# Kernel tuning notes

Hardware: AMD Instinct MI355X
Metric: run time of the kernel (lower is better)

Reference implementation:

```python
import jax, jax.numpy as jnp
import numpy as np
from jax import lax

KERNEL = 3
SAMPLING_RATE = 100.0
N_GRID = 201  # np.linspace(-1, 1, 201) sub-sample grid


def setup_inputs() -> dict:
    key = jax.random.key(0)
    nb, nc, nx, nt = 32, 3, 64, 4096
    xcorr = jax.random.normal(key, (nb, nc, nx, nt), dtype=jnp.float32)
    return {"xcorr": xcorr, "nlag": nt // 2}


def reference(xcorr, nlag):
    nt = xcorr.shape[-1]
    x = jnp.abs(xcorr)  # vabs=True

    # max_pool2d with (1, kernel=3), stride 1, padding (0, 1) -> SAME max over lag axis
    smax = lax.reduce_window(
        x, -jnp.inf, lax.max,
        window_dimensions=(1, 1, 1, KERNEL),
        window_strides=(1, 1, 1, 1),
        padding=[(0, 0), (0, 0), (0, 0), (KERNEL // 2, KERNEL // 2)],
    )
    keep = (smax == x).astype(x.dtype)

    # top-2 local maxima along lag axis (sorted descending, like torch.topk)
    topk_score, topk_idx = lax.top_k(x * keep, 2)
    s0 = topk_score[..., 0]
    s1 = topk_score[..., 1]
    weight = (0.1 + 3.0 * (s0 - s1)) * s0 ** 2
    i0 = topk_idx[..., 0]  # [nb, nc, nx]

    # --- sub-sample interpolation: 3-point spline == parabola through neighbors ---
    offsets = jnp.array([-1, 0, 1], dtype=i0.dtype)
    nbr_idx = jnp.clip(i0[..., None] + offsets, 0, nt - 1)      # [nb,nc,nx,3]
    y = jnp.take_along_axis(x, nbr_idx, axis=-1)                 # [nb,nc,nx,3]
    ym1, y0, yp1 = y[..., 0], y[..., 1], y[..., 2]
    a = 0.5 * (ym1 + yp1) - y0   # quadratic coeff
    b = 0.5 * (yp1 - ym1)        # linear coeff
    c = y0                       # constant

    xg = jnp.linspace(-1.0, 1.0, N_GRID, dtype=x.dtype)          # [201]
    yg = (a[..., None] * xg + b[..., None]) * xg + c[..., None]  # [nb,nc,nx,201]
    ii = jnp.argmax(yg, axis=-1)                                  # [nb,nc,nx]
    sub_shift = xg[ii]
    topk_idx_f = i0.astype(x.dtype) + sub_shift
    topk_score0 = jnp.take_along_axis(yg, ii[..., None], axis=-1)[..., 0]

    # pick the channel with the largest weight
    idx = jnp.argmax(weight, axis=1, keepdims=True)               # [nb,1,nx]
    max_cc = jnp.take_along_axis(topk_score0, idx, axis=1)
    w = jnp.take_along_axis(weight, idx, axis=1)
    shift_idx = jnp.take_along_axis(topk_idx_f, idx, axis=1) - jnp.asarray(nlag, x.dtype)
    shift_t = shift_idx / SAMPLING_RATE

    # stacked: [cc_max, cc_weight, cc_dt, cc_shift], each [nb,1,nx]
    return jnp.stack([max_cc, w, shift_t, shift_idx], axis=0)
```

## Files before the change

### kernel.cpp

```cpp
#include <hip/hip_runtime.h>
#include <math.h>

#define NB 32
#define NC 3
#define NX 64
#define NT 4096
#define NROWS (NB * NC * NX)

struct Quad { float4 a, b, c, d; };

__device__ __forceinline__ Quad load_chunk(const float* __restrict__ xr,
                                           int coff, int lane) {
    const float* base = xr + (size_t)coff + (size_t)(lane << 2);
    Quad q;
    q.a = *reinterpret_cast<const float4*>(base);
    q.b = *reinterpret_cast<const float4*>(base + 256);
    q.c = *reinterpret_cast<const float4*>(base + 512);
    q.d = *reinterpret_cast<const float4*>(base + 768);
    return q;
}

__device__ __forceinline__ void proc4(float a0, float a1, float a2, float a3,
                                      float cl, float cr, int t4,
                                      float& v0, int& i0, float& v1)
{
    const float c0 = (a0 >= cl && a0 >= a1) ? a0 : 0.0f;
    const float c1 = (a1 >= a0 && a1 >= a2) ? a1 : 0.0f;
    const float c2 = (a2 >= a1 && a2 >= a3) ? a2 : 0.0f;
    const float c3 = (a3 >= a2 && a3 >= cr) ? a3 : 0.0f;
    bool g;
    g = c0 > v0; v1 = g ? v0 : fmaxf(v1, c0); v0 = fmaxf(v0, c0); i0 = g ? t4     : i0;
    g = c1 > v0; v1 = g ? v0 : fmaxf(v1, c1); v0 = fmaxf(v0, c1); i0 = g ? t4 + 1 : i0;
    g = c2 > v0; v1 = g ? v0 : fmaxf(v1, c2); v0 = fmaxf(v0, c2); i0 = g ? t4 + 2 : i0;
    g = c3 > v0; v1 = g ? v0 : fmaxf(v1, c3); v0 = fmaxf(v0, c3); i0 = g ? t4 + 3 : i0;
}

__device__ __forceinline__ void scan_chunk(Quad q, float lmf, float rmf,
                                           int coff, int lane,
                                           float& v0, int& i0, float& v1)
{
    const int base = coff + (lane << 2);

    const float a00 = fabsf(q.a.x), a01 = fabsf(q.a.y), a02 = fabsf(q.a.z), a03 = fabsf(q.a.w);
    const float a10 = fabsf(q.b.x), a11 = fabsf(q.b.y), a12 = fabsf(q.b.z), a13 = fabsf(q.b.w);
    const float a20 = fabsf(q.c.x), a21 = fabsf(q.c.y), a22 = fabsf(q.c.z), a23 = fabsf(q.c.w);
    const float a30 = fabsf(q.d.x), a31 = fabsf(q.d.y), a32 = fabsf(q.d.z), a33 = fabsf(q.d.w);

    float lm, rm, t;

    lm = __shfl_up(a03, 1);
    lm = (lane == 0) ? lmf : lm;
    rm = __shfl_down(a00, 1);
    t  = __shfl(a10, 0);
    rm = (lane == 63) ? t : rm;
    proc4(a00, a01, a02, a03, lm, rm, base, v0, i0, v1);

    lm = __shfl_up(a13, 1);
    t  = __shfl(a03, 63);
    lm = (lane == 0) ? t : lm;
    rm = __shfl_down(a10, 1);
    t  = __shfl(a20, 0);
    rm = (lane == 63) ? t : rm;
    proc4(a10, a11, a12, a13, lm, rm, base + 256, v0, i0, v1);

    lm = __shfl_up(a23, 1);
    t  = __shfl(a13, 63);
    lm = (lane == 0) ? t : lm;
    rm = __shfl_down(a20, 1);
    t  = __shfl(a30, 0);
    rm = (lane == 63) ? t : rm;
    proc4(a20, a21, a22, a23, lm, rm, base + 512, v0, i0, v1);

    lm = __shfl_up(a33, 1);
    t  = __shfl(a23, 63);
    lm = (lane == 0) ? t : lm;
    rm = __shfl_down(a30, 1);
    rm = (lane == 63) ? rmf : rm;
    proc4(a30, a31, a32, a33, lm, rm, base + 768, v0, i0, v1);
}

__global__ __launch_bounds__(256) void scan_rows_kernel(
    const float* __restrict__ xcorr,
    float* __restrict__ wsv0, int* __restrict__ wsi0, float* __restrict__ wsv1)
{
    const int tid  = threadIdx.x;
    const int lane = tid & 63;
    const int wid  = tid >> 6;
    const int row  = blockIdx.x * 4 + wid;

    const float* __restrict__ xr = xcorr + (size_t)row * NT;

    float v0 = -1.0f, v1 = -1.0f; int i0 = 0;
    float pl, nf;

    Quad qA = load_chunk(xr, 0, lane);
    Quad qB = load_chunk(xr, 1024, lane);

    nf = __shfl(fabsf(qB.a.x), 0);
    scan_chunk(qA, -INFINITY, nf, 0, lane, v0, i0, v1);
    pl = __shfl(fabsf(qA.d.w), 63);

    qA = load_chunk(xr, 2048, lane);
    nf = __shfl(fabsf(qA.a.x), 0);
    scan_chunk(qB, pl, nf, 1024, lane, v0, i0, v1);
    pl = __shfl(fabsf(qB.d.w), 63);

    qB = load_chunk(xr, 3072, lane);
    nf = __shfl(fabsf(qB.a.x), 0);
    scan_chunk(qA, pl, nf, 2048, lane, v0, i0, v1);
    pl = __shfl(fabsf(qA.d.w), 63);

    scan_chunk(qB, pl, -INFINITY, 3072, lane, v0, i0, v1);

    #pragma unroll
    for (int off = 1; off < 64; off <<= 1) {
        const float ov0 = __shfl_xor(v0, off);
        const int   oi0 = __shfl_xor(i0, off);
        const float ov1 = __shfl_xor(v1, off);
        const bool big = (ov0 > v0) || (ov0 == v0 && oi0 < i0);
        const float loser = big ? v0 : ov0;
        v1 = fmaxf(fmaxf(v1, ov1), loser);
        v0 = big ? ov0 : v0;
        i0 = big ? oi0 : i0;
    }

    if (lane == 0) {
        wsv0[row] = v0;
        wsi0[row] = i0;
        wsv1[row] = v1;
    }
}

__global__ __launch_bounds__(256) void epilogue_kernel(
    const float* __restrict__ xcorr,
    const float* __restrict__ wsv0, const int* __restrict__ wsi0,
    const float* __restrict__ wsv1,
    const int*   __restrict__ nlag_p,
    float* __restrict__ out)
{
    const int g = blockIdx.x * 256 + threadIdx.x;
    if (g >= NB * NX) return;
    const int b = g >> 6;
    const int x = g & 63;

    const int r0 = (b * NC + 0) * NX + x;
    const int r1 = (b * NC + 1) * NX + x;
    const int r2 = (b * NC + 2) * NX + x;

    const float m00 = wsv0[r0], m10 = wsv1[r0]; const int p0 = wsi0[r0];
    const float m01 = wsv0[r1], m11 = wsv1[r1]; const int p1 = wsi0[r1];
    const float m02 = wsv0[r2], m12 = wsv1[r2]; const int p2 = wsi0[r2];

    const float w0 = (0.1f + 3.0f * (m00 - m10)) * (m00 * m00);
    const float w1 = (0.1f + 3.0f * (m01 - m11)) * (m01 * m01);
    const float w2 = (0.1f + 3.0f * (m02 - m12)) * (m02 * m02);

    const bool t1 = w1 > w0;
    float bw = t1 ? w1 : w0;
    float bs = t1 ? m01 : m00;
    int   bp = t1 ? p1 : p0;
    int   rs = t1 ? r1 : r0;
    const bool t2 = w2 > bw;
    bw = t2 ? w2 : bw;
    bs = t2 ? m02 : bs;
    bp = t2 ? p2 : bp;
    rs = t2 ? r2 : rs;

    const float* __restrict__ xrs = xcorr + (size_t)rs * NT;

    const float ym1 = fabsf(xrs[bp > 0 ? bp - 1 : 0]);
    const float yp1 = fabsf(xrs[bp < NT - 1 ? bp + 1 : NT - 1]);
    const float A = 0.5f * (ym1 + yp1) - bs;
    const float B = 0.5f * (yp1 - ym1);
    const float C = bs;

    int gi; float bv;
    if (A == 0.0f) {
        gi = (B > 0.0f) ? 200 : 0;
        const float xg = 0.01f * (float)(gi - 100);
        bv = (A * xg + B) * xg + C;
    } else {
        float gv = (1.0f - 0.5f * B / A) * 100.0f;
        gv = fminf(fmaxf(gv, 0.0f), 200.0f);
        const int glo = (int)gv;
        bv = -INFINITY; gi = 0;
        #pragma unroll
        for (int d = -1; d <= 2; ++d) {
            int gg = glo + d;
            gg = gg < 0 ? 0 : (gg > 200 ? 200 : gg);
            const float xg = 0.01f * (float)(gg - 100);
            const float yg = (A * xg + B) * xg + C;
            if (yg > bv) { bv = yg; gi = gg; }
        }
    }

    const float fidx = (float)bp + 0.01f * (float)(gi - 100);
    const float nlagf = (float)(*nlag_p);
    const float shift_idx = fidx - nlagf;
    const int n = NB * NX;
    out[0 * n + g] = bv;
    out[1 * n + g] = bw;
    out[2 * n + g] = shift_idx / 100.0f;
    out[3 * n + g] = shift_idx;
}

extern "C" void kernel_launch(void* const* d_in, const int* in_sizes, int n_in,
                              void* d_out, int out_size, void* d_ws, size_t ws_size,
                              hipStream_t stream) {
    const float* xcorr  = (const float*)d_in[0];
    const int*   nlag_p = (const int*)d_in[1];
    float* out = (float*)d_out;

    float* ws   = (float*)d_ws;
    float* wsv0 = ws;
    int*   wsi0 = (int*)(ws + NROWS);
    float* wsv1 = ws + 2 * NROWS;

    scan_rows_kernel<<<NROWS / 4, 256, 0, stream>>>(xcorr, wsv0, wsi0, wsv1);

    epilogue_kernel<<<(NB * NX + 255) / 256, 256, 0, stream>>>(
        xcorr, wsv0, wsi0, wsv1, nlag_p, out);
}
```

Measured before the change: 25.01 us.

## Give each lane 16 contiguous samples and split top-2 accumulators into four chains

Each lane now loads 16 contiguous floats per 1024-sample chunk instead of four strided float4s. This drops most cross-lane shuffles for neighbor values to one shuffle up and one down per chunk. All four chunks are loaded up front, and each chunk keeps its own top-2 accumulator so the dependency chains are independent; the accumulators are merged at the end. Lanes now read 64-byte contiguous segments rather than fully coalesced 16-byte strided ones, and holding all four chunks in flight raises register pressure.

```diff
diff --git a/kernel.cpp b/kernel.cpp
--- a/kernel.cpp
+++ b/kernel.cpp
@@ -9,74 +9,71 @@
 
 struct Quad { float4 a, b, c, d; };
 
-__device__ __forceinline__ Quad load_chunk(const float* __restrict__ xr,
-                                           int coff, int lane) {
-    const float* base = xr + (size_t)coff + (size_t)(lane << 2);
+__device__ __forceinline__ Quad load_chunk16(const float* __restrict__ xr,
+                                             int coff, int lane) {
+    const float* base = xr + (size_t)coff + (size_t)(lane << 4);
     Quad q;
     q.a = *reinterpret_cast<const float4*>(base);
-    q.b = *reinterpret_cast<const float4*>(base + 256);
-    q.c = *reinterpret_cast<const float4*>(base + 512);
-    q.d = *reinterpret_cast<const float4*>(base + 768);
+    q.b = *reinterpret_cast<const float4*>(base + 4);
+    q.c = *reinterpret_cast<const float4*>(base + 8);
+    q.d = *reinterpret_cast<const float4*>(base + 12);
     return q;
 }
 
-__device__ __forceinline__ void proc4(float a0, float a1, float a2, float a3,
-                                      float cl, float cr, int t4,
-                                      float& v0, int& i0, float& v1)
-{
-    const float c0 = (a0 >= cl && a0 >= a1) ? a0 : 0.0f;
-    const float c1 = (a1 >= a0 && a1 >= a2) ? a1 : 0.0f;
-    const float c2 = (a2 >= a1 && a2 >= a3) ? a2 : 0.0f;
-    const float c3 = (a3 >= a2 && a3 >= cr) ? a3 : 0.0f;
-    bool g;
-    g = c0 > v0; v1 = g ? v0 : fmaxf(v1, c0); v0 = fmaxf(v0, c0); i0 = g ? t4     : i0;
-    g = c1 > v0; v1 = g ? v0 : fmaxf(v1, c1); v0 = fmaxf(v0, c1); i0 = g ? t4 + 1 : i0;
-    g = c2 > v0; v1 = g ? v0 : fmaxf(v1, c2); v0 = fmaxf(v0, c2); i0 = g ? t4 + 2 : i0;
-    g = c3 > v0; v1 = g ? v0 : fmaxf(v1, c3); v0 = fmaxf(v0, c3); i0 = g ? t4 + 3 : i0;
-}
-
-__device__ __forceinline__ void scan_chunk(Quad q, float lmf, float rmf,
-                                           int coff, int lane,
-                                           float& v0, int& i0, float& v1)
-{
-    const int base = coff + (lane << 2);
-
-    const float a00 = fabsf(q.a.x), a01 = fabsf(q.a.y), a02 = fabsf(q.a.z), a03 = fabsf(q.a.w);
-    const float a10 = fabsf(q.b.x), a11 = fabsf(q.b.y), a12 = fabsf(q.b.z), a13 = fabsf(q.b.w);
-    const float a20 = fabsf(q.c.x), a21 = fabsf(q.c.y), a22 = fabsf(q.c.z), a23 = fabsf(q.c.w);
-    const float a30 = fabsf(q.d.x), a31 = fabsf(q.d.y), a32 = fabsf(q.d.z), a33 = fabsf(q.d.w);
-
-    float lm, rm, t;
-
-    lm = __shfl_up(a03, 1);
-    lm = (lane == 0) ? lmf : lm;
-    rm = __shfl_down(a00, 1);
-    t  = __shfl(a10, 0);
-    rm = (lane == 63) ? t : rm;
-    proc4(a00, a01, a02, a03, lm, rm, base, v0, i0, v1);
-
-    lm = __shfl_up(a13, 1);
-    t  = __shfl(a03, 63);
-    lm = (lane == 0) ? t : lm;
-    rm = __shfl_down(a10, 1);
-    t  = __shfl(a20, 0);
-    rm = (lane == 63) ? t : rm;
-    proc4(a10, a11, a12, a13, lm, rm, base + 256, v0, i0, v1);
-
-    lm = __shfl_up(a23, 1);
-    t  = __shfl(a13, 63);
-    lm = (lane == 0) ? t : lm;
-    rm = __shfl_down(a20, 1);
-    t  = __shfl(a30, 0);
-    rm = (lane == 63) ? t : rm;
-    proc4(a20, a21, a22, a23, lm, rm, base + 512, v0, i0, v1);
-
-    lm = __shfl_up(a33, 1);
-    t  = __shfl(a23, 63);
-    lm = (lane == 0) ? t : lm;
-    rm = __shfl_down(a30, 1);
-    rm = (lane == 63) ? rmf : rm;
-    proc4(a30, a31, a32, a33, lm, rm, base + 768, v0, i0, v1);
+__device__ __forceinline__ float keep3(float l, float x, float r) {
+    const float m = fmaxf(fmaxf(l, x), r);
+    return (x == m) ? x : 0.0f;
+}
+
+__device__ __forceinline__ void ins(float c, int t, float& m0, int& i0, float& m1) {
+    const bool g = c > m0;
+    m1 = g ? m0 : fmaxf(m1, c);
+    m0 = fmaxf(m0, c);
+    i0 = g ? t : i0;
+}
+
+__device__ __forceinline__ void scan_chunk16(Quad q, float lmE, float rmE,
+                                             int coff, int lane,
+                                             float& m0, int& i0, float& m1)
+{
+    const int tb = coff + (lane << 4);
+
+    const float e0  = fabsf(q.a.x), e1  = fabsf(q.a.y), e2  = fabsf(q.a.z), e3  = fabsf(q.a.w);
+    const float e4  = fabsf(q.b.x), e5  = fabsf(q.b.y), e6  = fabsf(q.b.z), e7  = fabsf(q.b.w);
+    const float e8  = fabsf(q.c.x), e9  = fabsf(q.c.y), e10 = fabsf(q.c.z), e11 = fabsf(q.c.w);
+    const float e12 = fabsf(q.d.x), e13 = fabsf(q.d.y), e14 = fabsf(q.d.z), e15 = fabsf(q.d.w);
+
+    float lm = __shfl_up(e15, 1);
+    lm = (lane == 0) ? lmE : lm;
+    float rm = __shfl_down(e0, 1);
+    rm = (lane == 63) ? rmE : rm;
+
+    ins(keep3(lm,  e0,  e1 ), tb + 0,  m0, i0, m1);
+    ins(keep3(e0,  e1,  e2 ), tb + 1,  m0, i0, m1);
+    ins(keep3(e1,  e2,  e3 ), tb + 2,  m0, i0, m1);
+    ins(keep3(e2,  e3,  e4 ), tb + 3,  m0, i0, m1);
+    ins(keep3(e3,  e4,  e5 ), tb + 4,  m0, i0, m1);
+    ins(keep3(e4,  e5,  e6 ), tb + 5,  m0, i0, m1);
+    ins(keep3(e5,  e6,  e7 ), tb + 6,  m0, i0, m1);
+    ins(keep3(e6,  e7,  e8 ), tb + 7,  m0, i0, m1);
+    ins(keep3(e7,  e8,  e9 ), tb + 8,  m0, i0, m1);
+    ins(keep3(e8,  e9,  e10), tb + 9,  m0, i0, m1);
+    ins(keep3(e9,  e10, e11), tb + 10, m0, i0, m1);
+    ins(keep3(e10, e11, e12), tb + 11, m0, i0, m1);
+    ins(keep3(e11, e12, e13), tb + 12, m0, i0, m1);
+    ins(keep3(e12, e13, e14), tb + 13, m0, i0, m1);
+    ins(keep3(e13, e14, e15), tb + 14, m0, i0, m1);
+    ins(keep3(e14, e15, rm ), tb + 15, m0, i0, m1);
+}
+
+__device__ __forceinline__ void merge_acc(float& m0, int& i0, float& m1,
+                                          float bm0, int bi0, float bm1)
+{
+    const bool big = bm0 > m0;
+    const float loser = big ? m0 : bm0;
+    m1 = fmaxf(fmaxf(m1, bm1), loser);
+    m0 = big ? bm0 : m0;
+    i0 = big ? bi0 : i0;
 }
 
 __global__ __launch_bounds__(256) void scan_rows_kernel(
@@ -90,27 +87,34 @@
 
     const float* __restrict__ xr = xcorr + (size_t)row * NT;
 
-    float v0 = -1.0f, v1 = -1.0f; int i0 = 0;
-    float pl, nf;
-
-    Quad qA = load_chunk(xr, 0, lane);
-    Quad qB = load_chunk(xr, 1024, lane);
-
-    nf = __shfl(fabsf(qB.a.x), 0);
-    scan_chunk(qA, -INFINITY, nf, 0, lane, v0, i0, v1);
-    pl = __shfl(fabsf(qA.d.w), 63);
-
-    qA = load_chunk(xr, 2048, lane);
-    nf = __shfl(fabsf(qA.a.x), 0);
-    scan_chunk(qB, pl, nf, 1024, lane, v0, i0, v1);
-    pl = __shfl(fabsf(qB.d.w), 63);
-
-    qB = load_chunk(xr, 3072, lane);
-    nf = __shfl(fabsf(qB.a.x), 0);
-    scan_chunk(qA, pl, nf, 2048, lane, v0, i0, v1);
-    pl = __shfl(fabsf(qA.d.w), 63);
-
-    scan_chunk(qB, pl, -INFINITY, 3072, lane, v0, i0, v1);
+    float m0a = -1.0f, m1a = -1.0f; int i0a = 0;
+    float m0b = -1.0f, m1b = -1.0f; int i0b = 0;
+    float m0c = -1.0f, m1c = -1.0f; int i0c = 0;
+    float m0d = -1.0f, m1d = -1.0f; int i0d = 0;
+
+    Quad q0 = load_chunk16(xr, 0,    lane);
+    Quad q1 = load_chunk16(xr, 1024, lane);
+
+    Quad q2 = load_chunk16(xr, 2048, lane);
+    float nf = __shfl(fabsf(q1.a.x), 0);
+    scan_chunk16(q0, -INFINITY, nf, 0, lane, m0a, i0a, m1a);
+    float pl = __shfl(fabsf(q0.d.w), 63);
+
+    Quad q3 = load_chunk16(xr, 3072, lane);
+    nf = __shfl(fabsf(q2.a.x), 0);
+    scan_chunk16(q1, pl, nf, 1024, lane, m0b, i0b, m1b);
+    pl = __shfl(fabsf(q1.d.w), 63);
+
+    nf = __shfl(fabsf(q3.a.x), 0);
+    scan_chunk16(q2, pl, nf, 2048, lane, m0c, i0c, m1c);
+    pl = __shfl(fabsf(q2.d.w), 63);
+
+    scan_chunk16(q3, pl, -INFINITY, 3072, lane, m0d, i0d, m1d);
+
+    merge_acc(m0a, i0a, m1a, m0b, i0b, m1b);
+    merge_acc(m0c, i0c, m1c, m0d, i0d, m1d);
+    merge_acc(m0a, i0a, m1a, m0c, i0c, m1c);
+    float v0 = m0a, v1 = m1a; int i0 = i0a;
 
     #pragma unroll
     for (int off = 1; off < 64; off <<= 1) {
```

Result: no change. 24.76 us (-1.0%).
